# Kernel tuning notes

Measured on AMD Instinct MI355X. Metric: run time of the kernel, lower is better.

## Reference

```python
import jax, jax.numpy as jnp
import numpy as np

D_MODEL = 1024
NUM_LAYERS = 4
VOCAB = 32000
NUM_HEADS = 8
HEAD_DIM = D_MODEL // NUM_HEADS
FFN_DIM = 2048
BATCH = 4
SEQ = 1024
LN_EPS = 1e-5
ROPE_THETA = 10000.0


def setup_inputs() -> dict:
    key = jax.random.key(0)
    ks = iter(jax.random.split(key, 32))
    std = 0.02
    L, D, H, Dh, F, V = NUM_LAYERS, D_MODEL, NUM_HEADS, HEAD_DIM, FFN_DIM, VOCAB
    inp = {
        "tokens": jax.random.randint(next(ks), (BATCH, SEQ), 0, V, dtype=jnp.int32),
        "emb": jax.random.normal(next(ks), (V, D), jnp.float32),
        # per-layer stacked params; Linear weights stored pre-transposed (in, out)
        "Wqkv": jax.random.normal(next(ks), (L, D, 3 * D), jnp.float32) * std,
        "bqkv": jnp.zeros((L, 3 * D), jnp.float32),
        "Wo": jax.random.normal(next(ks), (L, D, D), jnp.float32) * std,
        "bo": jnp.zeros((L, D), jnp.float32),
        "ln1_g": jnp.ones((L, D), jnp.float32),
        "ln1_b": jnp.zeros((L, D), jnp.float32),
        "ln2_g": jnp.ones((L, D), jnp.float32),
        "ln2_b": jnp.zeros((L, D), jnp.float32),
        "W1": jax.random.normal(next(ks), (L, D, F), jnp.float32) * std,
        "b1": jnp.zeros((L, F), jnp.float32),
        "W2": jax.random.normal(next(ks), (L, F, D), jnp.float32) * std,
        "b2": jnp.zeros((L, D), jnp.float32),
        "lnf_g": jnp.ones((D,), jnp.float32),
        "lnf_b": jnp.zeros((D,), jnp.float32),
        "Wout": jax.random.normal(next(ks), (D, V), jnp.float32) * std,
        "bout": jnp.zeros((V,), jnp.float32),
    }
    return inp


def _layernorm(x, g, b):
    mu = jnp.mean(x, -1, keepdims=True)
    var = jnp.mean(jnp.square(x - mu), -1, keepdims=True)
    return (x - mu) * jax.lax.rsqrt(var + LN_EPS) * g + b


def _rope_cos_sin(seq, dh, dtype):
    inv_freq = 1.0 / (ROPE_THETA ** (jnp.arange(0, dh, 2, dtype=jnp.float32) / dh))
    t = jnp.arange(seq, dtype=jnp.float32)
    freqs = jnp.outer(t, inv_freq)                      # [S, Dh/2]
    emb = jnp.concatenate([freqs, freqs], axis=-1)      # [S, Dh]
    return jnp.cos(emb).astype(dtype), jnp.sin(emb).astype(dtype)


def _rotate_half(x):
    x1, x2 = jnp.split(x, 2, axis=-1)
    return jnp.concatenate([-x2, x1], axis=-1)


def _apply_rope(x, cos, sin):
    # x: [B,S,H,Dh]; cos/sin: [S,Dh] -> broadcast over batch and heads
    return x * cos[None, :, None, :] + _rotate_half(x) * sin[None, :, None, :]


def reference(tokens, emb, Wqkv, bqkv, Wo, bo, ln1_g, ln1_b, ln2_g, ln2_b,
              W1, b1, W2, b2, lnf_g, lnf_b, Wout, bout):
    B, S = tokens.shape
    H, Dh = NUM_HEADS, HEAD_DIM
    x = emb[tokens]                                      # [B,S,D]
    cos, sin = _rope_cos_sin(S, Dh, x.dtype)
    causal = jnp.tril(jnp.ones((S, S), dtype=bool))      # True = keep
    scale = 1.0 / jnp.sqrt(jnp.asarray(Dh, x.dtype))

    def layer(xc, p):
        (wqkv, bq, wo, bo_, g1, b1_, g2, b2_, w1, bb1, w2, bb2) = p
        y = _layernorm(xc, g1, b1_)
        qkv = (y @ wqkv + bq).reshape(B, S, 3, H, Dh)
        q, k, v = qkv[:, :, 0], qkv[:, :, 1], qkv[:, :, 2]
        q = _apply_rope(q, cos, sin)
        k = _apply_rope(k, cos, sin)
        scores = jnp.einsum("bshd,bthd->bhst", q, k) * scale
        scores = jnp.where(causal[None, None], scores, -jnp.inf)
        attn = jax.nn.softmax(scores, axis=-1)
        ctx = jnp.einsum("bhst,bthd->bshd", attn, v).reshape(B, S, H * Dh)
        xc = xc + ctx @ wo + bo_
        z = _layernorm(xc, g2, b2_)
        ff = jax.nn.gelu(z @ w1 + bb1, approximate=False) @ w2 + bb2
        return xc + ff, None

    params = (Wqkv, bqkv, Wo, bo, ln1_g, ln1_b, ln2_g, ln2_b, W1, b1, W2, b2)
    x, _ = jax.lax.scan(layer, x, params)
    x = _layernorm(x, lnf_g, lnf_b)
    return x @ Wout + bout                                # [B,S,V]
```

## Files before the change

### kernel.cpp

```cpp
#include <hip/hip_runtime.h>
#include <hip/hip_bf16.h>
#include <math.h>


#define D_MODEL 1024
#define SEQ     1024
#define BATCH   4
#define NHEAD   8
#define HDIM    128
#define FFN     2048
#define NLAYER  4
#define VOCAB   32000
#define MROWS   (BATCH*SEQ)

typedef unsigned short ushort_t;
typedef __attribute__((ext_vector_type(8))) short s16x8;
typedef __attribute__((ext_vector_type(4))) float f32x4;

__device__ __forceinline__ ushort_t f2bf(float f) {
    union { float f; unsigned int u; } c; c.f = f;
    unsigned int u = c.u;
    unsigned int r = (u + 0x7FFFu + ((u >> 16) & 1u)) >> 16;
    return (ushort_t)r;
}
__device__ __forceinline__ float bf2f(ushort_t u) {
    union { unsigned int u; float f; } c; c.u = ((unsigned int)u) << 16; return c.f;
}

__device__ __forceinline__ void gload16(const void* g, void* l) {
    __builtin_amdgcn_global_load_lds(
        (const __attribute__((address_space(1))) unsigned int*)g,
        (__attribute__((address_space(3))) unsigned int*)l, 16, 0, 0);
}

__device__ __forceinline__ float gelu_exact(float x) {
    return 0.5f * x * (1.0f + erff(x * 0.70710678118654752f));
}

__global__ __launch_bounds__(256) void embed_kernel(
    const int* __restrict__ tokens, const float* __restrict__ emb,
    float* __restrict__ X)
{
    int row = blockIdx.x;
    int t = tokens[row];
    const float4* src = (const float4*)(emb + (size_t)t * D_MODEL);
    float4* dst = (float4*)(X + (size_t)row * D_MODEL);
    dst[threadIdx.x] = src[threadIdx.x];
}

__global__ __launch_bounds__(256) void ln_kernel(
    const float* __restrict__ X, const float* __restrict__ g,
    const float* __restrict__ b, ushort_t* __restrict__ Y)
{
    __shared__ float red[8];
    int row = blockIdx.x;
    const float4* x4 = (const float4*)(X + (size_t)row * D_MODEL);
    float4 v = x4[threadIdx.x];
    float s  = v.x + v.y + v.z + v.w;
    float ss = v.x*v.x + v.y*v.y + v.z*v.z + v.w*v.w;
    #pragma unroll
    for (int o = 32; o > 0; o >>= 1) { s += __shfl_down(s, o); ss += __shfl_down(ss, o); }
    int wid = threadIdx.x >> 6;
    if ((threadIdx.x & 63) == 0) { red[wid] = s; red[wid + 4] = ss; }
    __syncthreads();
    float tot  = red[0] + red[1] + red[2] + red[3];
    float tot2 = red[4] + red[5] + red[6] + red[7];
    float mu  = tot * (1.0f / D_MODEL);
    float var = tot2 * (1.0f / D_MODEL) - mu * mu;
    float r = rsqrtf(var + 1e-5f);
    const float4* g4 = (const float4*)g;
    const float4* b4 = (const float4*)b;
    float4 gv = g4[threadIdx.x], bv = b4[threadIdx.x];
    ushort4 o;
    o.x = f2bf((v.x - mu) * r * gv.x + bv.x);
    o.y = f2bf((v.y - mu) * r * gv.y + bv.y);
    o.z = f2bf((v.z - mu) * r * gv.z + bv.z);
    o.w = f2bf((v.w - mu) * r * gv.w + bv.w);
    ((ushort4*)(Y + (size_t)row * D_MODEL))[threadIdx.x] = o;
}

__global__ __launch_bounds__(256) void wconv(
    const float* __restrict__ W, ushort_t* __restrict__ Wt, int K, int N)
{
    __shared__ float t[32][33];
    const float* Wl = W + (size_t)blockIdx.z * K * N;
    ushort_t* Wtl = Wt + (size_t)blockIdx.z * K * N;
    int k0 = blockIdx.y * 32, n0 = blockIdx.x * 32;
    int tid = threadIdx.x;
    int r = tid >> 3, c4 = (tid & 7) * 4;
    float4 v = *(const float4*)(Wl + (size_t)(k0 + r) * N + n0 + c4);
    t[r][c4+0] = v.x; t[r][c4+1] = v.y; t[r][c4+2] = v.z; t[r][c4+3] = v.w;
    __syncthreads();
    ushort4 o;
    o.x = f2bf(t[c4+0][r]); o.y = f2bf(t[c4+1][r]);
    o.z = f2bf(t[c4+2][r]); o.w = f2bf(t[c4+3][r]);
    *(ushort4*)(Wtl + (size_t)(n0 + r) * K + k0 + c4) = o;
}

template<int ACT, int BETA, int OBF>
__global__ __launch_bounds__(256) void gemm_mid(
    const ushort_t* __restrict__ A, const ushort_t* __restrict__ Bt,
    const float* __restrict__ bias, float* __restrict__ Cf,
    ushort_t* __restrict__ Cb, int M, int N, int K)
{
    __shared__ __align__(16) ushort_t As[2][128 * 64];
    __shared__ __align__(16) ushort_t Bs[2][128 * 64];
    int tid = threadIdx.x, lane = tid & 63, w = tid >> 6;
    int wm = w >> 1, wn = w & 1;
    int m0 = blockIdx.x * 128, n0 = blockIdx.y * 128;
    int lr = lane & 15, kg = lane >> 4;
    const int NKT = K / 64;

    f32x4 acc[4][4] = {};

    int srow = w * 8 + (lane >> 3);
    int scol = (((lane & 7) ^ ((lane >> 3) & 7))) * 8;

    int rsw = lr & 7;
    int ch0 = (kg    ) ^ rsw;
    int ch1 = (kg + 4) ^ rsw;

#define STAGE_A(db, ht, ktile) do { \
    const ushort_t* s_ = A + (size_t)(m0 + (ht) * 64 + srow) * K + (size_t)(ktile) * 64 + scol; \
    gload16(s_,                  &As[db][((ht) * 64 + w * 8) * 64]); \
    gload16(s_ + (size_t)32 * K, &As[db][((ht) * 64 + 32 + w * 8) * 64]); \
} while (0)
#define STAGE_B(db, ht, ktile) do { \
    const ushort_t* s_ = Bt + (size_t)(n0 + (ht) * 64 + srow) * K + (size_t)(ktile) * 64 + scol; \
    gload16(s_,                  &Bs[db][((ht) * 64 + w * 8) * 64]); \
    gload16(s_ + (size_t)32 * K, &Bs[db][((ht) * 64 + 32 + w * 8) * 64]); \
} while (0)
#define SBAR() do { __builtin_amdgcn_sched_barrier(0); \
    __builtin_amdgcn_s_barrier(); __builtin_amdgcn_sched_barrier(0); } while (0)

    STAGE_A(0, 0, 0); STAGE_A(0, 1, 0); STAGE_B(0, 0, 0); STAGE_B(0, 1, 0);
    STAGE_A(1, 0, 1);
    asm volatile("s_waitcnt vmcnt(2)" ::: "memory");
    SBAR();

    for (int kt = 0; kt < NKT; ++kt) {
        int d = kt & 1, dn = d ^ 1;
        const ushort_t* pa0 = &As[d][(wm * 64 + lr) * 64 + ch0 * 8];
        const ushort_t* pa1 = &As[d][(wm * 64 + lr) * 64 + ch1 * 8];
        const ushort_t* pb0 = &Bs[d][(wn * 64 + lr) * 64 + ch0 * 8];
        const ushort_t* pb1 = &Bs[d][(wn * 64 + lr) * 64 + ch1 * 8];
        s16x8 a[4][2], b[4][2];

        #pragma unroll
        for (int mi = 0; mi < 4; ++mi) {
            a[mi][0] = *(const s16x8*)(pa0 + mi * 1024);
            a[mi][1] = *(const s16x8*)(pa1 + mi * 1024);
        }
        #pragma unroll
        for (int ni = 0; ni < 4; ++ni) {
            b[ni][0] = *(const s16x8*)(pb0 + ni * 1024);
            b[ni][1] = *(const s16x8*)(pb1 + ni * 1024);
        }
        if (kt + 1 < NKT) STAGE_A(dn, 1, kt + 1);
        __builtin_amdgcn_sched_barrier(0);

        __builtin_amdgcn_s_setprio(1);
        #pragma unroll
        for (int mi = 0; mi < 2; ++mi)
            #pragma unroll
            for (int ni = 0; ni < 2; ++ni)
                #pragma unroll
                for (int kk = 0; kk < 2; ++kk)
                    acc[mi][ni] = __builtin_amdgcn_mfma_f32_16x16x32_bf16(
                        a[mi][kk], b[ni][kk], acc[mi][ni], 0, 0, 0);
        __builtin_amdgcn_s_setprio(0);
        __builtin_amdgcn_sched_barrier(0);
        if (kt + 1 < NKT) STAGE_B(dn, 0, kt + 1);
        __builtin_amdgcn_sched_barrier(0);

        __builtin_amdgcn_s_setprio(1);
        #pragma unroll
        for (int mi = 0; mi < 2; ++mi)
            #pragma unroll
            for (int ni = 2; ni < 4; ++ni)
                #pragma unroll
                for (int kk = 0; kk < 2; ++kk)
                    acc[mi][ni] = __builtin_amdgcn_mfma_f32_16x16x32_bf16(
                        a[mi][kk], b[ni][kk], acc[mi][ni], 0, 0, 0);
        __builtin_amdgcn_s_setprio(0);
        __builtin_amdgcn_sched_barrier(0);
        if (kt + 1 < NKT) STAGE_B(dn, 1, kt + 1);
        __builtin_amdgcn_sched_barrier(0);

        __builtin_amdgcn_s_setprio(1);
        #pragma unroll
        for (int mi = 2; mi < 4; ++mi)
            #pragma unroll
            for (int ni = 0; ni < 2; ++ni)
                #pragma unroll
                for (int kk = 0; kk < 2; ++kk)
                    acc[mi][ni] = __builtin_amdgcn_mfma_f32_16x16x32_bf16(
                        a[mi][kk], b[ni][kk], acc[mi][ni], 0, 0, 0);
        __builtin_amdgcn_s_setprio(0);

        asm volatile("s_waitcnt lgkmcnt(0)" ::: "memory");
        SBAR();
        if (kt + 2 < NKT) STAGE_A(d, 0, kt + 2);
        __builtin_amdgcn_sched_barrier(0);

        __builtin_amdgcn_s_setprio(1);
        #pragma unroll
        for (int mi = 2; mi < 4; ++mi)
            #pragma unroll
            for (int ni = 2; ni < 4; ++ni)
                #pragma unroll
                for (int kk = 0; kk < 2; ++kk)
                    acc[mi][ni] = __builtin_amdgcn_mfma_f32_16x16x32_bf16(
                        a[mi][kk], b[ni][kk], acc[mi][ni], 0, 0, 0);
        __builtin_amdgcn_s_setprio(0);

        if (kt + 2 < NKT) {
            asm volatile("s_waitcnt vmcnt(2)" ::: "memory");
        } else {
            asm volatile("s_waitcnt vmcnt(0)" ::: "memory");
        }
        SBAR();
    }
#undef STAGE_A
#undef STAGE_B
#undef SBAR

    #pragma unroll
    for (int mi = 0; mi < 4; ++mi) {
        int rbase = m0 + wm * 64 + mi * 16 + kg * 4;
        #pragma unroll
        for (int ni = 0; ni < 4; ++ni) {
            int col = n0 + wn * 64 + ni * 16 + lr;
            float bz = bias[col];
            f32x4 v = acc[mi][ni];
            #pragma unroll
            for (int j = 0; j < 4; ++j) {
                float x = v[j] + bz;
                if (ACT == 1) x = gelu_exact(x);
                size_t off = (size_t)(rbase + j) * N + col;
                if (OBF) {
                    Cb[off] = f2bf(x);
                } else {
                    if (BETA) x += Cf[off];
                    Cf[off] = x;
                }
            }
        }
    }
}

__global__ __launch_bounds__(512) void gemm_big(
    const ushort_t* __restrict__ A, const ushort_t* __restrict__ Bt,
    const float* __restrict__ bias, float* __restrict__ C,
    int M, int N, int K)
{
    __shared__ __align__(16) ushort_t As[2][256 * 64];
    __shared__ __align__(16) ushort_t Bs[2][256 * 64];
    int tid = threadIdx.x, lane = tid & 63, w = tid >> 6;
    int wm = w >> 2, wn = w & 3;
    int m0 = blockIdx.x * 256, n0 = blockIdx.y * 256;
    int lr = lane & 15, kg = lane >> 4;
    const int NKT = K / 64;

    f32x4 acc[8][4] = {};

    int srow = w * 8 + (lane >> 3);
    int scol = (((lane & 7) ^ ((lane >> 3) & 7))) * 8;

    int rsw = lr & 7;
    int ch0 = (kg    ) ^ rsw;
    int ch1 = (kg + 4) ^ rsw;

#define STAGE_A(db, ht, ktile) do { \
    const ushort_t* s_ = A + (size_t)(m0 + (ht) * 128 + srow) * K + (size_t)(ktile) * 64 + scol; \
    gload16(s_,                  &As[db][((ht) * 128 + w * 8) * 64]); \
    gload16(s_ + (size_t)64 * K, &As[db][((ht) * 128 + 64 + w * 8) * 64]); \
} while (0)
#define STAGE_B(db, ht, ktile) do { \
    const ushort_t* s_ = Bt + (size_t)(n0 + (ht) * 128 + srow) * K + (size_t)(ktile) * 64 + scol; \
    gload16(s_,                  &Bs[db][((ht) * 128 + w * 8) * 64]); \
    gload16(s_ + (size_t)64 * K, &Bs[db][((ht) * 128 + 64 + w * 8) * 64]); \
} while (0)
#define SBAR() do { __builtin_amdgcn_sched_barrier(0); \
    __builtin_amdgcn_s_barrier(); __builtin_amdgcn_sched_barrier(0); } while (0)

    STAGE_A(0, 0, 0); STAGE_A(0, 1, 0); STAGE_B(0, 0, 0); STAGE_B(0, 1, 0);
    STAGE_A(1, 0, 1);
    asm volatile("s_waitcnt vmcnt(2)" ::: "memory");
    SBAR();

    for (int kt = 0; kt < NKT; ++kt) {
        int d = kt & 1, dn = d ^ 1;
        const ushort_t* pa0 = &As[d][(wm * 128 + lr) * 64 + ch0 * 8];
        const ushort_t* pa1 = &As[d][(wm * 128 + lr) * 64 + ch1 * 8];
        const ushort_t* pb0 = &Bs[d][(wn * 64  + lr) * 64 + ch0 * 8];
        const ushort_t* pb1 = &Bs[d][(wn * 64  + lr) * 64 + ch1 * 8];
        s16x8 a03[4][2], a47[4][2], b01[2][2], b23[2][2];

        #pragma unroll
        for (int mi = 0; mi < 4; ++mi) {
            a03[mi][0] = *(const s16x8*)(pa0 + mi * 1024);
            a03[mi][1] = *(const s16x8*)(pa1 + mi * 1024);
        }
        #pragma unroll
        for (int ni = 0; ni < 2; ++ni) {
            b01[ni][0] = *(const s16x8*)(pb0 + ni * 1024);
            b01[ni][1] = *(const s16x8*)(pb1 + ni * 1024);
        }
        #pragma unroll
        for (int ni = 0; ni < 2; ++ni) {
            b23[ni][0] = *(const s16x8*)(pb0 + (2 + ni) * 1024);
            b23[ni][1] = *(const s16x8*)(pb1 + (2 + ni) * 1024);
        }
        #pragma unroll
        for (int mi = 0; mi < 4; ++mi) {
            a47[mi][0] = *(const s16x8*)(pa0 + (4 + mi) * 1024);
            a47[mi][1] = *(const s16x8*)(pa1 + (4 + mi) * 1024);
        }
        if (kt + 1 < NKT) STAGE_A(dn, 1, kt + 1);
        __builtin_amdgcn_sched_barrier(0);

        __builtin_amdgcn_s_setprio(1);
        #pragma unroll
        for (int mi = 0; mi < 4; ++mi)
            #pragma unroll
            for (int ni = 0; ni < 2; ++ni)
                #pragma unroll
                for (int kk = 0; kk < 2; ++kk)
                    acc[mi][ni] = __builtin_amdgcn_mfma_f32_16x16x32_bf16(
                        a03[mi][kk], b01[ni][kk], acc[mi][ni], 0, 0, 0);
        __builtin_amdgcn_s_setprio(0);
        __builtin_amdgcn_sched_barrier(0);
        if (kt + 1 < NKT) STAGE_B(dn, 0, kt + 1);
        __builtin_amdgcn_sched_barrier(0);

        __builtin_amdgcn_s_setprio(1);
        #pragma unroll
        for (int mi = 0; mi < 4; ++mi)
            #pragma unroll
            for (int ni = 0; ni < 2; ++ni)
                #pragma unroll
                for (int kk = 0; kk < 2; ++kk)
                    acc[mi][2 + ni] = __builtin_amdgcn_mfma_f32_16x16x32_bf16(
                        a03[mi][kk], b23[ni][kk], acc[mi][2 + ni], 0, 0, 0);
        __builtin_amdgcn_s_setprio(0);
        __builtin_amdgcn_sched_barrier(0);
        if (kt + 1 < NKT) STAGE_B(dn, 1, kt + 1);
        __builtin_amdgcn_sched_barrier(0);

        __builtin_amdgcn_s_setprio(1);
        #pragma unroll
        for (int mi = 0; mi < 4; ++mi)
            #pragma unroll
            for (int ni = 0; ni < 2; ++ni)
                #pragma unroll
                for (int kk = 0; kk < 2; ++kk)
                    acc[4 + mi][ni] = __builtin_amdgcn_mfma_f32_16x16x32_bf16(
                        a47[mi][kk], b01[ni][kk], acc[4 + mi][ni], 0, 0, 0);
        __builtin_amdgcn_s_setprio(0);

        asm volatile("s_waitcnt lgkmcnt(0)" ::: "memory");
        SBAR();
        if (kt + 2 < NKT) STAGE_A(d, 0, kt + 2);
        __builtin_amdgcn_sched_barrier(0);

        __builtin_amdgcn_s_setprio(1);
        #pragma unroll
        for (int mi = 0; mi < 4; ++mi)
            #pragma unroll
            for (int ni = 0; ni < 2; ++ni)
                #pragma unroll
                for (int kk = 0; kk < 2; ++kk)
                    acc[4 + mi][2 + ni] = __builtin_amdgcn_mfma_f32_16x16x32_bf16(
                        a47[mi][kk], b23[ni][kk], acc[4 + mi][2 + ni], 0, 0, 0);
        __builtin_amdgcn_s_setprio(0);

        if (kt + 2 < NKT) {
            asm volatile("s_waitcnt vmcnt(2)" ::: "memory");
        } else {
            asm volatile("s_waitcnt vmcnt(0)" ::: "memory");
        }
        SBAR();
    }
#undef STAGE_A
#undef STAGE_B
#undef SBAR

    #pragma unroll
    for (int mi = 0; mi < 8; ++mi) {
        int rbase = m0 + wm * 128 + mi * 16 + kg * 4;
        #pragma unroll
        for (int ni = 0; ni < 4; ++ni) {
            int col = n0 + wn * 64 + ni * 16 + lr;
            float bz = bias[col];
            f32x4 v = acc[mi][ni];
            #pragma unroll
            for (int j = 0; j < 4; ++j)
                C[(size_t)(rbase + j) * N + col] = v[j] + bz;
        }
    }
}

__global__ __launch_bounds__(64) void rope_table_kernel(float2* __restrict__ RT)
{
    int s = blockIdx.x, p = threadIdx.x;
    float inv = expf(-0.14391156831212788f * (float)p);
    float ang = (float)s * inv;
    float sn, c;
    sincosf(ang, &sn, &c);
    RT[s * 64 + p] = make_float2(c, sn);
}

__global__ __launch_bounds__(256) void ropeq_kernel(
    const ushort_t* __restrict__ QKVb, const float2* __restrict__ RT,
    ushort_t* __restrict__ Qb, ushort_t* __restrict__ Kb)
{
    int m = blockIdx.x;
    int b = m >> 10, s = m & (SEQ - 1);
    const ushort_t* rowbase = QKVb + (size_t)m * (3 * D_MODEL);
    const float2* t2 = RT + s * 64;
    int tid = threadIdx.x;
    int qk = tid >> 7;
    int rem = tid & 127;
    int hh = rem >> 4;
    int p4 = (rem & 15) * 4;
    const ushort_t* base = rowbase + qk * D_MODEL + hh * HDIM + p4;
    ushort4 lo = *(const ushort4*)base;
    ushort4 hi = *(const ushort4*)(base + 64);
    ushort_t lov[4] = {lo.x, lo.y, lo.z, lo.w};
    ushort_t hiv[4] = {hi.x, hi.y, hi.z, hi.w};
    ushort_t lor[4], hir[4];
    #pragma unroll
    for (int j = 0; j < 4; ++j) {
        float2 cs = t2[p4 + j];
        float x1 = bf2f(lov[j]), x2 = bf2f(hiv[j]);
        lor[j] = f2bf(x1 * cs.x - x2 * cs.y);
        hir[j] = f2bf(x2 * cs.x + x1 * cs.y);
    }
    ushort_t* dst = (qk ? Kb : Qb) + ((size_t)(b * NHEAD + hh) * SEQ + s) * HDIM + p4;
    *(ushort4*)dst        = make_ushort4(lor[0], lor[1], lor[2], lor[3]);
    *(ushort4*)(dst + 64) = make_ushort4(hir[0], hir[1], hir[2], hir[3]);
}

__global__ __launch_bounds__(256) void vtrans_kernel(
    const ushort_t* __restrict__ QKVb, ushort_t* __restrict__ Vt)
{
    __shared__ ushort_t tl[64][34];
    int s0 = blockIdx.x * 64;
    int d0 = blockIdx.y * 32;
    int b  = blockIdx.z;
    int tid = threadIdx.x;
    #pragma unroll
    for (int r = 0; r < 4; ++r) {
        int li = tid + r * 256;
        int row = li >> 4;
        int cp  = (li & 15) * 2;
        ushort2 v = *(const ushort2*)(QKVb + (size_t)(b * SEQ + s0 + row) * 3072
                                      + 2 * D_MODEL + d0 + cp);
        tl[row][cp]     = v.x;
        tl[row][cp + 1] = v.y;
    }
    __syncthreads();
    #pragma unroll
    for (int r = 0; r < 4; ++r) {
        int li = tid + r * 256;
        int drow = li >> 5;
        int sc   = (li & 31) * 2;
        ushort2 o;
        o.x = tl[sc][drow];
        o.y = tl[sc + 1][drow];
        *(ushort2*)(Vt + (size_t)(b * D_MODEL + d0 + drow) * SEQ + s0 + sc) = o;
    }
}

#define PSTR 72

__global__ __launch_bounds__(256) void attn_mfma(
    const ushort_t* __restrict__ Qb, const ushort_t* __restrict__ Kb,
    const ushort_t* __restrict__ Vt, ushort_t* __restrict__ Yb)
{
    __shared__ __align__(16) ushort_t Ks[64 * 136];
    __shared__ __align__(16) ushort_t Vts[128 * 72];
    __shared__ __align__(16) ushort_t Pl[4][16 * PSTR];
    int bid = blockIdx.x;
    int sflip = ((bid >> 8) ^ bid) & 1;
    int h4 = (bid >> 1) & 15;
    int qt = sflip ? 15 - h4 : h4;
    int bh = ((bid & 1) << 4) | ((bid >> 5) & 15);
    int b = bh >> 3, h = bh & 7;
    int q0 = qt * 64;
    int tid = threadIdx.x, lane = tid & 63, w = tid >> 6;
    int lr = lane & 15, g = lane >> 4;
    const float scale = 0.08838834764831845f;

    const ushort_t* Qbase = Qb + (size_t)((b * NHEAD + h) * SEQ) * HDIM;
    const ushort_t* Kbase = Kb + (size_t)((b * NHEAD + h) * SEQ) * HDIM;
    const ushort_t* Vbase = Vt + (size_t)(b * D_MODEL + h * HDIM) * SEQ;

    s16x8 aq[4];
    #pragma unroll
    for (int kc = 0; kc < 4; ++kc)
        aq[kc] = *(const s16x8*)(Qbase + (size_t)(q0 + w * 16 + lr) * HDIM + kc * 32 + g * 8);

    int krow = tid >> 4, kc16 = tid & 15;
    int vrow = tid >> 3, vc8  = tid & 7;

    f32x4 acc_o[8] = {};
    float mx[4] = {-INFINITY, -INFINITY, -INFINITY, -INFINITY};
    float ls[4] = {};

    s16x8 kreg[4], vreg[4];
    #pragma unroll
    for (int r = 0; r < 4; ++r)
        kreg[r] = *(const s16x8*)(Kbase + (size_t)(krow + r * 16) * HDIM + kc16 * 8);
    #pragma unroll
    for (int r = 0; r < 4; ++r)
        vreg[r] = *(const s16x8*)(Vbase + (size_t)(vrow + r * 32) * SEQ + vc8 * 8);

    int ntiles = q0 / 64 + 1;
    for (int t = 0; t < ntiles; ++t) {
        int j0 = t * 64;
        __syncthreads();
        #pragma unroll
        for (int r = 0; r < 4; ++r)
            *(s16x8*)&Ks[(krow + r * 16) * 136 + kc16 * 8] = kreg[r];
        #pragma unroll
        for (int r = 0; r < 4; ++r)
            *(s16x8*)&Vts[(vrow + r * 32) * 72 + vc8 * 8] = vreg[r];
        if (t + 1 < ntiles) {
            int jn = j0 + 64;
            #pragma unroll
            for (int r = 0; r < 4; ++r)
                kreg[r] = *(const s16x8*)(Kbase + (size_t)(jn + krow + r * 16) * HDIM + kc16 * 8);
            #pragma unroll
            for (int r = 0; r < 4; ++r)
                vreg[r] = *(const s16x8*)(Vbase + (size_t)(vrow + r * 32) * SEQ + jn + vc8 * 8);
        }
        __syncthreads();

        f32x4 sa[4] = {};
        __builtin_amdgcn_s_setprio(1);
        #pragma unroll
        for (int nb = 0; nb < 4; ++nb)
            #pragma unroll
            for (int kc = 0; kc < 4; ++kc) {
                s16x8 bk = *(const s16x8*)&Ks[(nb * 16 + lr) * 136 + kc * 32 + g * 8];
                sa[nb] = __builtin_amdgcn_mfma_f32_16x16x32_bf16(aq[kc], bk, sa[nb], 0, 0, 0);
            }
        __builtin_amdgcn_s_setprio(0);

        bool diag = (j0 == q0);
        float pv[4][4];
        #pragma unroll
        for (int nb = 0; nb < 4; ++nb)
            #pragma unroll
            for (int j = 0; j < 4; ++j) {
                float v = sa[nb][j] * scale;
                if (diag) {
                    int kv = j0 + nb * 16 + lr;
                    int qq = q0 + w * 16 + g * 4 + j;
                    if (kv > qq) v = -INFINITY;
                }
                pv[nb][j] = v;
            }
        #pragma unroll
        for (int j = 0; j < 4; ++j) {
            float tm = fmaxf(fmaxf(pv[0][j], pv[1][j]), fmaxf(pv[2][j], pv[3][j]));
            #pragma unroll
            for (int o = 1; o < 16; o <<= 1) tm = fmaxf(tm, __shfl_xor(tm, o));
            if (tm > mx[j] + 8.0f) {
                float corr = expf(mx[j] - tm);
                mx[j] = tm;
                ls[j] *= corr;
                #pragma unroll
                for (int dn = 0; dn < 8; ++dn) acc_o[dn][j] *= corr;
            }
            float ts = 0.0f;
            #pragma unroll
            for (int nb = 0; nb < 4; ++nb) {
                float e = expf(pv[nb][j] - mx[j]);
                pv[nb][j] = e;
                ts += e;
            }
            #pragma unroll
            for (int o = 1; o < 16; o <<= 1) ts += __shfl_xor(ts, o);
            ls[j] += ts;
        }
        #pragma unroll
        for (int nb = 0; nb < 4; ++nb)
            #pragma unroll
            for (int j = 0; j < 4; ++j)
                Pl[w][(g * 4 + j) * PSTR + nb * 16 + lr] = f2bf(pv[nb][j]);
        #pragma unroll
        for (int kk = 0; kk < 2; ++kk) {
            s16x8 pa = *(const s16x8*)&Pl[w][lr * PSTR + kk * 32 + g * 8];
            __builtin_amdgcn_s_setprio(1);
            #pragma unroll
            for (int dn = 0; dn < 8; ++dn) {
                s16x8 bv = *(const s16x8*)&Vts[(dn * 16 + lr) * 72 + kk * 32 + g * 8];
                acc_o[dn] = __builtin_amdgcn_mfma_f32_16x16x32_bf16(pa, bv, acc_o[dn], 0, 0, 0);
            }
            __builtin_amdgcn_s_setprio(0);
        }
    }

    float il[4];
    #pragma unroll
    for (int j = 0; j < 4; ++j) il[j] = 1.0f / ls[j];
    #pragma unroll
    for (int dn = 0; dn < 8; ++dn)
        #pragma unroll
        for (int j = 0; j < 4; ++j) {
            int q = q0 + w * 16 + g * 4 + j;
            Yb[(size_t)(b * SEQ + q) * D_MODEL + h * HDIM + dn * 16 + lr] =
                f2bf(acc_o[dn][j] * il[j]);
        }
}

extern "C" void kernel_launch(void* const* d_in, const int* in_sizes, int n_in,
                              void* d_out, int out_size, void* d_ws, size_t ws_size,
                              hipStream_t stream)
{
    const int*   tokens = (const int*)  d_in[0];
    const float* emb    = (const float*)d_in[1];
    const float* Wqkv   = (const float*)d_in[2];
    const float* bqkv   = (const float*)d_in[3];
    const float* Wo     = (const float*)d_in[4];
    const float* bo     = (const float*)d_in[5];
    const float* ln1_g  = (const float*)d_in[6];
    const float* ln1_b  = (const float*)d_in[7];
    const float* ln2_g  = (const float*)d_in[8];
    const float* ln2_b  = (const float*)d_in[9];
    const float* W1     = (const float*)d_in[10];
    const float* b1     = (const float*)d_in[11];
    const float* W2     = (const float*)d_in[12];
    const float* b2     = (const float*)d_in[13];
    const float* lnf_g  = (const float*)d_in[14];
    const float* lnf_b  = (const float*)d_in[15];
    const float* Wout   = (const float*)d_in[16];
    const float* bout   = (const float*)d_in[17];
    float* out = (float*)d_out;

    char* ws = (char*)d_ws;
    float*    X      = (float*)ws;
    ushort_t* Abuf   = (ushort_t*)(ws + 16777216);
    ushort_t* QKVb   = (ushort_t*)(ws + 25165824);
    ushort_t* Gbuf   = (ushort_t*)(ws + 25165824);
    ushort_t* Qbb    = (ushort_t*)(ws + 50331648);
    ushort_t* Kbb    = (ushort_t*)(ws + 58720256);
    ushort_t* Vtb    = (ushort_t*)(ws + 67108864);
    ushort_t* WqkvT  = (ushort_t*)(ws + 75497472);
    ushort_t* WoT    = (ushort_t*)(ws + 100663296);
    ushort_t* W1T    = (ushort_t*)(ws + 109051904);
    ushort_t* W2T    = (ushort_t*)(ws + 125829120);
    ushort_t* WoutT  = (ushort_t*)(ws + 142606336);
    float2*   RT     = (float2*)  (ws + 208142336);

    const int M = MROWS, Dm = D_MODEL, F = FFN, V = VOCAB;

    rope_table_kernel<<<SEQ, 64, 0, stream>>>(RT);

    wconv<<<dim3(3*Dm/32, Dm/32, NLAYER), 256, 0, stream>>>(Wqkv, WqkvT, Dm, 3*Dm);
    wconv<<<dim3(Dm/32,   Dm/32, NLAYER), 256, 0, stream>>>(Wo,   WoT,   Dm, Dm);
    wconv<<<dim3(F/32,    Dm/32, NLAYER), 256, 0, stream>>>(W1,   W1T,   Dm, F);
    wconv<<<dim3(Dm/32,   F/32,  NLAYER), 256, 0, stream>>>(W2,   W2T,   F,  Dm);
    wconv<<<dim3(V/32,    Dm/32, 1),      256, 0, stream>>>(Wout, WoutT, Dm, V);

    embed_kernel<<<MROWS, 256, 0, stream>>>(tokens, emb, X);

    for (int L = 0; L < NLAYER; ++L) {
        ln_kernel<<<MROWS, 256, 0, stream>>>(X, ln1_g + (size_t)L*Dm, ln1_b + (size_t)L*Dm, Abuf);
        gemm_mid<0,0,1><<<dim3(M/128, 3*Dm/128), 256, 0, stream>>>(
            Abuf, WqkvT + (size_t)L*3*Dm*Dm, bqkv + (size_t)L*3*Dm, nullptr, QKVb, M, 3*Dm, Dm);
        ropeq_kernel<<<MROWS, 256, 0, stream>>>(QKVb, RT, Qbb, Kbb);
        vtrans_kernel<<<dim3(SEQ/64, Dm/32, BATCH), 256, 0, stream>>>(QKVb, Vtb);
        attn_mfma<<<BATCH*NHEAD*(SEQ/64), 256, 0, stream>>>(Qbb, Kbb, Vtb, Abuf);
        gemm_mid<0,1,0><<<dim3(M/128, Dm/128), 256, 0, stream>>>(
            Abuf, WoT + (size_t)L*Dm*Dm, bo + (size_t)L*Dm, X, nullptr, M, Dm, Dm);
        ln_kernel<<<MROWS, 256, 0, stream>>>(X, ln2_g + (size_t)L*Dm, ln2_b + (size_t)L*Dm, Abuf);
        gemm_mid<1,0,1><<<dim3(M/128, F/128), 256, 0, stream>>>(
            Abuf, W1T + (size_t)L*Dm*F, b1 + (size_t)L*F, nullptr, Gbuf, M, F, Dm);
        gemm_mid<0,1,0><<<dim3(M/128, Dm/128), 256, 0, stream>>>(
            Gbuf, W2T + (size_t)L*F*Dm, b2 + (size_t)L*Dm, X, nullptr, M, Dm, F);
    }

    ln_kernel<<<MROWS, 256, 0, stream>>>(X, lnf_g, lnf_b, Abuf);
    gemm_big<<<dim3(M/256, V/256), 512, 0, stream>>>(
        Abuf, WoutT, bout, out, M, V, Dm);
}
```

Before: 1.349 ms.

## Give each attention wave two 16-row query groups with 128-thread blocks

```diff
diff --git a/kernel.cpp b/kernel.cpp
--- a/kernel.cpp
+++ b/kernel.cpp
@@ -475,13 +475,13 @@
 
 #define PSTR 72
 
-__global__ __launch_bounds__(256) void attn_mfma(
+__global__ __launch_bounds__(128) void attn_mfma(
     const ushort_t* __restrict__ Qb, const ushort_t* __restrict__ Kb,
     const ushort_t* __restrict__ Vt, ushort_t* __restrict__ Yb)
 {
     __shared__ __align__(16) ushort_t Ks[64 * 136];
     __shared__ __align__(16) ushort_t Vts[128 * 72];
-    __shared__ __align__(16) ushort_t Pl[4][16 * PSTR];
+    __shared__ __align__(16) ushort_t Pl[2][32 * PSTR];
     int bid = blockIdx.x;
     int sflip = ((bid >> 8) ^ bid) & 1;
     int h4 = (bid >> 1) & 15;
@@ -497,124 +497,148 @@
     const ushort_t* Kbase = Kb + (size_t)((b * NHEAD + h) * SEQ) * HDIM;
     const ushort_t* Vbase = Vt + (size_t)(b * D_MODEL + h * HDIM) * SEQ;
 
-    s16x8 aq[4];
-    #pragma unroll
-    for (int kc = 0; kc < 4; ++kc)
-        aq[kc] = *(const s16x8*)(Qbase + (size_t)(q0 + w * 16 + lr) * HDIM + kc * 32 + g * 8);
+    s16x8 aq[2][4];
+    #pragma unroll
+    for (int rg = 0; rg < 2; ++rg)
+        #pragma unroll
+        for (int kc = 0; kc < 4; ++kc)
+            aq[rg][kc] = *(const s16x8*)(Qbase
+                + (size_t)(q0 + w * 32 + rg * 16 + lr) * HDIM + kc * 32 + g * 8);
 
     int krow = tid >> 4, kc16 = tid & 15;
     int vrow = tid >> 3, vc8  = tid & 7;
 
-    f32x4 acc_o[8] = {};
-    float mx[4] = {-INFINITY, -INFINITY, -INFINITY, -INFINITY};
-    float ls[4] = {};
-
-    s16x8 kreg[4], vreg[4];
-    #pragma unroll
-    for (int r = 0; r < 4; ++r)
-        kreg[r] = *(const s16x8*)(Kbase + (size_t)(krow + r * 16) * HDIM + kc16 * 8);
-    #pragma unroll
-    for (int r = 0; r < 4; ++r)
-        vreg[r] = *(const s16x8*)(Vbase + (size_t)(vrow + r * 32) * SEQ + vc8 * 8);
+    f32x4 acc_o[2][8] = {};
+    float mx[2][4] = {{-INFINITY,-INFINITY,-INFINITY,-INFINITY},
+                      {-INFINITY,-INFINITY,-INFINITY,-INFINITY}};
+    float ls[2][4] = {};
+
+    s16x8 kreg[8], vreg[8];
+    #pragma unroll
+    for (int r = 0; r < 8; ++r)
+        kreg[r] = *(const s16x8*)(Kbase + (size_t)(krow + r * 8) * HDIM + kc16 * 8);
+    #pragma unroll
+    for (int r = 0; r < 8; ++r)
+        vreg[r] = *(const s16x8*)(Vbase + (size_t)(vrow + r * 16) * SEQ + vc8 * 8);
 
     int ntiles = q0 / 64 + 1;
     for (int t = 0; t < ntiles; ++t) {
         int j0 = t * 64;
         __syncthreads();
         #pragma unroll
-        for (int r = 0; r < 4; ++r)
-            *(s16x8*)&Ks[(krow + r * 16) * 136 + kc16 * 8] = kreg[r];
-        #pragma unroll
-        for (int r = 0; r < 4; ++r)
-            *(s16x8*)&Vts[(vrow + r * 32) * 72 + vc8 * 8] = vreg[r];
+        for (int r = 0; r < 8; ++r)
+            *(s16x8*)&Ks[(krow + r * 8) * 136 + kc16 * 8] = kreg[r];
+        #pragma unroll
+        for (int r = 0; r < 8; ++r)
+            *(s16x8*)&Vts[(vrow + r * 16) * 72 + vc8 * 8] = vreg[r];
         if (t + 1 < ntiles) {
             int jn = j0 + 64;
             #pragma unroll
-            for (int r = 0; r < 4; ++r)
-                kreg[r] = *(const s16x8*)(Kbase + (size_t)(jn + krow + r * 16) * HDIM + kc16 * 8);
-            #pragma unroll
-            for (int r = 0; r < 4; ++r)
-                vreg[r] = *(const s16x8*)(Vbase + (size_t)(vrow + r * 32) * SEQ + jn + vc8 * 8);
+            for (int r = 0; r < 8; ++r)
+                kreg[r] = *(const s16x8*)(Kbase + (size_t)(jn + krow + r * 8) * HDIM + kc16 * 8);
+            #pragma unroll
+            for (int r = 0; r < 8; ++r)
+                vreg[r] = *(const s16x8*)(Vbase + (size_t)(vrow + r * 16) * SEQ + jn + vc8 * 8);
         }
         __syncthreads();
 
-        f32x4 sa[4] = {};
+        f32x4 sa[2][4] = {};
         __builtin_amdgcn_s_setprio(1);
         #pragma unroll
         for (int nb = 0; nb < 4; ++nb)
             #pragma unroll
             for (int kc = 0; kc < 4; ++kc) {
                 s16x8 bk = *(const s16x8*)&Ks[(nb * 16 + lr) * 136 + kc * 32 + g * 8];
-                sa[nb] = __builtin_amdgcn_mfma_f32_16x16x32_bf16(aq[kc], bk, sa[nb], 0, 0, 0);
+                #pragma unroll
+                for (int rg = 0; rg < 2; ++rg)
+                    sa[rg][nb] = __builtin_amdgcn_mfma_f32_16x16x32_bf16(
+                        aq[rg][kc], bk, sa[rg][nb], 0, 0, 0);
             }
         __builtin_amdgcn_s_setprio(0);
 
         bool diag = (j0 == q0);
-        float pv[4][4];
-        #pragma unroll
-        for (int nb = 0; nb < 4; ++nb)
+        float pv[2][4][4];
+        #pragma unroll
+        for (int rg = 0; rg < 2; ++rg)
+            #pragma unroll
+            for (int nb = 0; nb < 4; ++nb)
+                #pragma unroll
+                for (int j = 0; j < 4; ++j) {
+                    float v = sa[rg][nb][j] * scale;
+                    if (diag) {
+                        int kv = j0 + nb * 16 + lr;
+                        int qq = q0 + w * 32 + rg * 16 + g * 4 + j;
+                        if (kv > qq) v = -INFINITY;
+                    }
+                    pv[rg][nb][j] = v;
+                }
+        #pragma unroll
+        for (int rg = 0; rg < 2; ++rg)
             #pragma unroll
             for (int j = 0; j < 4; ++j) {
-                float v = sa[nb][j] * scale;
-                if (diag) {
-                    int kv = j0 + nb * 16 + lr;
-                    int qq = q0 + w * 16 + g * 4 + j;
-                    if (kv > qq) v = -INFINITY;
+                float tm = fmaxf(fmaxf(pv[rg][0][j], pv[rg][1][j]),
+                                 fmaxf(pv[rg][2][j], pv[rg][3][j]));
+                #pragma unroll
+                for (int o = 1; o < 16; o <<= 1) tm = fmaxf(tm, __shfl_xor(tm, o));
+                if (tm > mx[rg][j] + 8.0f) {
+                    float corr = expf(mx[rg][j] - tm);
+                    mx[rg][j] = tm;
+                    ls[rg][j] *= corr;
+                    #pragma unroll
+                    for (int dn = 0; dn < 8; ++dn) acc_o[rg][dn][j] *= corr;
                 }
-                pv[nb][j] = v;
+                float ts = 0.0f;
+                #pragma unroll
+                for (int nb = 0; nb < 4; ++nb) {
+                    float e = expf(pv[rg][nb][j] - mx[rg][j]);
+                    pv[rg][nb][j] = e;
+                    ts += e;
+                }
+                #pragma unroll
+                for (int o = 1; o < 16; o <<= 1) ts += __shfl_xor(ts, o);
+                ls[rg][j] += ts;
             }
         #pragma unroll
-        for (int j = 0; j < 4; ++j) {
-            float tm = fmaxf(fmaxf(pv[0][j], pv[1][j]), fmaxf(pv[2][j], pv[3][j]));
-            #pragma unroll
-            for (int o = 1; o < 16; o <<= 1) tm = fmaxf(tm, __shfl_xor(tm, o));
-            if (tm > mx[j] + 8.0f) {
-                float corr = expf(mx[j] - tm);
-                mx[j] = tm;
-                ls[j] *= corr;
-                #pragma unroll
-                for (int dn = 0; dn < 8; ++dn) acc_o[dn][j] *= corr;
-            }
-            float ts = 0.0f;
-            #pragma unroll
-            for (int nb = 0; nb < 4; ++nb) {
-                float e = expf(pv[nb][j] - mx[j]);
-                pv[nb][j] = e;
-                ts += e;
-            }
-            #pragma unroll
-            for (int o = 1; o < 16; o <<= 1) ts += __shfl_xor(ts, o);
-            ls[j] += ts;
-        }
-        #pragma unroll
-        for (int nb = 0; nb < 4; ++nb)
-            #pragma unroll
-            for (int j = 0; j < 4; ++j)
-                Pl[w][(g * 4 + j) * PSTR + nb * 16 + lr] = f2bf(pv[nb][j]);
+        for (int rg = 0; rg < 2; ++rg)
+            #pragma unroll
+            for (int nb = 0; nb < 4; ++nb)
+                #pragma unroll
+                for (int j = 0; j < 4; ++j)
+                    Pl[w][(rg * 16 + g * 4 + j) * PSTR + nb * 16 + lr]
+                        = f2bf(pv[rg][nb][j]);
         #pragma unroll
         for (int kk = 0; kk < 2; ++kk) {
-            s16x8 pa = *(const s16x8*)&Pl[w][lr * PSTR + kk * 32 + g * 8];
+            s16x8 pa[2];
+            #pragma unroll
+            for (int rg = 0; rg < 2; ++rg)
+                pa[rg] = *(const s16x8*)&Pl[w][(rg * 16 + lr) * PSTR + kk * 32 + g * 8];
             __builtin_amdgcn_s_setprio(1);
             #pragma unroll
             for (int dn = 0; dn < 8; ++dn) {
                 s16x8 bv = *(const s16x8*)&Vts[(dn * 16 + lr) * 72 + kk * 32 + g * 8];
-                acc_o[dn] = __builtin_amdgcn_mfma_f32_16x16x32_bf16(pa, bv, acc_o[dn], 0, 0, 0);
+                #pragma unroll
+                for (int rg = 0; rg < 2; ++rg)
+                    acc_o[rg][dn] = __builtin_amdgcn_mfma_f32_16x16x32_bf16(
+                        pa[rg], bv, acc_o[rg][dn], 0, 0, 0);
             }
             __builtin_amdgcn_s_setprio(0);
         }
     }
 
-    float il[4];
-    #pragma unroll
-    for (int j = 0; j < 4; ++j) il[j] = 1.0f / ls[j];
-    #pragma unroll
-    for (int dn = 0; dn < 8; ++dn)
-        #pragma unroll
-        for (int j = 0; j < 4; ++j) {
-            int q = q0 + w * 16 + g * 4 + j;
-            Yb[(size_t)(b * SEQ + q) * D_MODEL + h * HDIM + dn * 16 + lr] =
-                f2bf(acc_o[dn][j] * il[j]);
-        }
+    #pragma unroll
+    for (int rg = 0; rg < 2; ++rg) {
+        float il[4];
+        #pragma unroll
+        for (int j = 0; j < 4; ++j) il[j] = 1.0f / ls[rg][j];
+        #pragma unroll
+        for (int dn = 0; dn < 8; ++dn)
+            #pragma unroll
+            for (int j = 0; j < 4; ++j) {
+                int q = q0 + w * 32 + rg * 16 + g * 4 + j;
+                Yb[(size_t)(b * SEQ + q) * D_MODEL + h * HDIM + dn * 16 + lr] =
+                    f2bf(acc_o[rg][dn][j] * il[j]);
+            }
+    }
 }
 
 extern "C" void kernel_launch(void* const* d_in, const int* in_sizes, int n_in,
@@ -674,7 +698,7 @@
             Abuf, WqkvT + (size_t)L*3*Dm*Dm, bqkv + (size_t)L*3*Dm, nullptr, QKVb, M, 3*Dm, Dm);
         ropeq_kernel<<<MROWS, 256, 0, stream>>>(QKVb, RT, Qbb, Kbb);
         vtrans_kernel<<<dim3(SEQ/64, Dm/32, BATCH), 256, 0, stream>>>(QKVb, Vtb);
-        attn_mfma<<<BATCH*NHEAD*(SEQ/64), 256, 0, stream>>>(Qbb, Kbb, Vtb, Abuf);
+        attn_mfma<<<BATCH*NHEAD*(SEQ/64), 128, 0, stream>>>(Qbb, Kbb, Vtb, Abuf);
         gemm_mid<0,1,0><<<dim3(M/128, Dm/128), 256, 0, stream>>>(
             Abuf, WoT + (size_t)L*Dm*Dm, bo + (size_t)L*Dm, X, nullptr, M, Dm, Dm);
         ln_kernel<<<MROWS, 256, 0, stream>>>(X, ln2_g + (size_t)L*Dm, ln2_b + (size_t)L*Dm, Abuf);
```

Measured after the change: 1.485 ms. +10.1%, slower.
